# Performance work log

Hardware: AMD Instinct MI355X
Metric: run time of the kernel (lower is better)

## Reference

```python
import jax, jax.numpy as jnp
import numpy as np

NOISE_LEVEL = 0.05
GAMMA = 0.2  # dt/tau


def setup_inputs() -> dict:
    key = jax.random.key(0)
    ks = jax.random.split(key, 4)
    B, T, I, L, O = 64, 512, 128, 1024, 128
    return {
        "input": jax.random.normal(ks[0], (B, T, I), dtype=jnp.float32),
        "noise": jax.random.normal(ks[1], (B, T, L), dtype=jnp.float32),
        "wi": jax.random.normal(ks[2], (I, L), dtype=jnp.float32),
        "si": jnp.ones((I,), dtype=jnp.float32),
        "wrec": jax.random.normal(ks[3], (L, L), dtype=jnp.float32) * (1.0 / np.sqrt(L)),
        "b": jnp.zeros((L,), dtype=jnp.float32),
        "wo": jax.random.normal(jax.random.fold_in(key, 7), (L, O), dtype=jnp.float32) * (1.0 / L),
        "so": jnp.ones((O,), dtype=jnp.float32),
        "h0": jnp.zeros((L,), dtype=jnp.float32),
    }


def reference(input, noise, wi, si, wrec, b, wo, so, h0):
    B = input.shape[0]
    # proxy parameters: wi_full = (wi.T * si).T == wi * si[:, None]; wo_full = wo * so
    wi_full = wi * si[:, None]          # (I, L)
    wo_full = wo * so                   # (L, O)

    h_init = jnp.broadcast_to(h0, (B, h0.shape[0]))  # (B, L)
    r_init = jnp.tanh(h_init)

    # Precompute input projections for all steps (no sequential dependency).
    u = jnp.einsum('bti,il->btl', input, wi_full)     # (B, T, L)

    def step(carry, xs):
        h, r = carry
        u_t, n_t = xs                                 # (B, L), (B, L)
        h = h + NOISE_LEVEL * n_t + GAMMA * (-h + r @ wrec.T + u_t)
        r = jnp.tanh(h + b)
        out_t = jnp.tanh(h) @ wo_full                 # (B, O)
        return (h, r), out_t

    xs = (jnp.swapaxes(u, 0, 1), jnp.swapaxes(noise, 0, 1))  # time-major
    _, out_t = jax.lax.scan(step, (h_init, r_init), xs)
    return jnp.swapaxes(out_t, 0, 1)                 # (B, T, O)
```

## Files before the change

kernel.cpp:

```cpp
#include <hip/hip_runtime.h>
#include <hip/hip_bf16.h>
#include <cstdint>
#include <cstddef>


static constexpr int B = 64, T = 512, I = 128, L = 1024, O = 128;
static constexpr float C_NOISE = 0.05f, C_GAMMA = 0.2f;

static constexpr int NROW = 4, BT = 16, NJB = 16, JT = 64;

static constexpr size_t WREC_OFF = 0;
static constexpr size_t WIT_OFF  = WREC_OFF + (size_t)L * L * 2;
static constexpr size_t WOT_OFF  = WIT_OFF + (size_t)L * I * 2;
static constexpr size_t RBUF_OFF = WOT_OFF + (size_t)O * L * 2;
static constexpr size_t RBUF_BYTES = (size_t)2 * B * L * 2;
static constexpr size_t HBUF_OFF = ((RBUF_OFF + RBUF_BYTES + 131072 + 511) / 512) * 512;
static constexpr size_t WS_NEED  = HBUF_OFF + (size_t)B * T * L * 2;

typedef __attribute__((ext_vector_type(8))) short s16x8;
typedef __attribute__((ext_vector_type(4))) float f32x4;
typedef __attribute__((ext_vector_type(2))) unsigned long long u64x2;

__device__ __forceinline__ float fexp2(float x) {
#if __has_builtin(__builtin_amdgcn_exp2f)
  return __builtin_amdgcn_exp2f(x);
#else
  return exp2f(x);
#endif
}
__device__ __forceinline__ float frcp(float x) {
#if __has_builtin(__builtin_amdgcn_rcpf)
  return __builtin_amdgcn_rcpf(x);
#else
  return 1.0f / x;
#endif
}
__device__ __forceinline__ float fast_tanh(float x) {
  float e = fexp2(x * 2.8853900817779268f);
  return 1.0f - 2.0f * frcp(e + 1.0f);
}
__device__ __forceinline__ uint16_t bf16bits(float x) {
  __hip_bfloat16 h = __float2bfloat16(x);
  return *reinterpret_cast<uint16_t*>(&h);
}

__global__ void pack_kernel(const float* __restrict__ wi, const float* __restrict__ si,
                            const float* __restrict__ wrec,
                            const float* __restrict__ wo, const float* __restrict__ so,
                            uint8_t* __restrict__ ws) {
  int idx = blockIdx.x * blockDim.x + threadIdx.x;
  int stride = gridDim.x * blockDim.x;

  __hip_bfloat16* wrecb = (__hip_bfloat16*)(ws + WREC_OFF);
  for (int i = idx; i < L * L; i += stride) wrecb[i] = __float2bfloat16(wrec[i]);

  __hip_bfloat16* wit = (__hip_bfloat16*)(ws + WIT_OFF);
  for (int n = idx; n < L * I; n += stride) {
    int l = n >> 7, ii = n & 127;
    wit[n] = __float2bfloat16(wi[(size_t)ii * L + l] * si[ii]);
  }
  __hip_bfloat16* wot = (__hip_bfloat16*)(ws + WOT_OFF);
  for (int n = idx; n < O * L; n += stride) {
    int o = n >> 10, l = n & 1023;
    wot[n] = __float2bfloat16(wo[(size_t)l * O + o] * so[o]);
  }
  uint32_t* rb = (uint32_t*)(ws + RBUF_OFF);
  for (size_t n = idx; n < RBUF_BYTES / 4; n += stride) rb[n] = 0;
}

__launch_bounds__(256, 1)
__global__ void rnn_kernel(const float* __restrict__ input, const float* __restrict__ noise,
                           const float* __restrict__ bvec, const float* __restrict__ h0,
                           uint8_t* __restrict__ ws) {
  const int tid  = threadIdx.x;
  const int lane = tid & 63;
  const int w    = tid >> 6;
  const int bx   = blockIdx.x;
  const int row  = bx & 3;
  const int jblk = bx >> 2;
  const int b0   = row * BT;
  const int j0   = jblk * JT;
  const int l15  = lane & 15;
  const int lhi  = lane >> 4;

  const int jc0  = j0 + w * 16 + lhi * 4;
  const int mybatch = b0 + l15;

  const short* wrecb = (const short*)(ws + WREC_OFF);
  const short* wit   = (const short*)(ws + WIT_OFF);
  uint64_t* rbuf     = (uint64_t*)(ws + RBUF_OFF);
  __hip_bfloat16* hbuf = (__hip_bfloat16*)(ws + HBUF_OFF);

  __shared__ __align__(16) uint8_t ldsA[2][16 * 2048];

  s16x8 wfrag[32];
  #pragma unroll
  for (int kt = 0; kt < 32; ++kt)
    wfrag[kt] = *(const s16x8*)(wrecb + (size_t)(j0 + w * 16 + l15) * L + kt * 32 + lhi * 8);
  s16x8 wifrag[4];
  #pragma unroll
  for (int kt = 0; kt < 4; ++kt)
    wifrag[kt] = *(const s16x8*)(wit + (size_t)(j0 + w * 16 + l15) * I + kt * 32 + lhi * 8);

  f32x4 bias, h;
  #pragma unroll
  for (int q = 0; q < 4; ++q) { bias[q] = bvec[jc0 + q]; h[q] = h0[jc0 + q]; }

  const int grow = tid >> 4;
  const int gseg = tid & 15;
  const int gsw  = (grow ^ gseg) & 7;

  {
    uint64_t pv = 0;
    #pragma unroll
    for (int q = 0; q < 4; ++q)
      pv |= (uint64_t)bf16bits(fast_tanh(h0[jc0 + q])) << (16 * q);
    pv = (pv & ~1ull) | 1ull;
    size_t slot = (size_t)mybatch * (L / 4) + (size_t)(jc0 >> 2);
    __hip_atomic_store(&rbuf[slot], pv, __ATOMIC_RELAXED, __HIP_MEMORY_SCOPE_AGENT);
  }

  for (int t = 0; t < T; ++t) {
    f32x4 inLo[4], inHi[4];
    #pragma unroll
    for (int kt = 0; kt < 4; ++kt) {
      const float* p = input + ((size_t)(b0 + l15) * T + t) * I + kt * 32 + lhi * 8;
      inLo[kt] = *(const f32x4*)p;
      inHi[kt] = *(const f32x4*)(p + 4);
    }
    f32x4 nz = *(const f32x4*)(noise + ((size_t)mybatch * T + t) * L + jc0);
    s16x8 af[4];
    #pragma unroll
    for (int kt = 0; kt < 4; ++kt)
      #pragma unroll
      for (int q = 0; q < 4; ++q) {
        af[kt][q]     = (short)bf16bits(inLo[kt][q]);
        af[kt][q + 4] = (short)bf16bits(inHi[kt][q]);
      }

    f32x4 acc0 = {0.f,0.f,0.f,0.f}, acc1 = {0.f,0.f,0.f,0.f};
    f32x4 acc2 = {0.f,0.f,0.f,0.f}, acc3 = {0.f,0.f,0.f,0.f};
    acc0 = __builtin_amdgcn_mfma_f32_16x16x32_bf16(wifrag[0], af[0], acc0, 0, 0, 0);
    acc1 = __builtin_amdgcn_mfma_f32_16x16x32_bf16(wifrag[1], af[1], acc1, 0, 0, 0);
    acc2 = __builtin_amdgcn_mfma_f32_16x16x32_bf16(wifrag[2], af[2], acc2, 0, 0, 0);
    acc3 = __builtin_amdgcn_mfma_f32_16x16x32_bf16(wifrag[3], af[3], acc3, 0, 0, 0);

    u64x2 v[8];
    {
      const uint64_t want = (uint64_t)(((t >> 1) & 1) ^ 1);
      const uint8_t* src = (const uint8_t*)rbuf
                         + (size_t)(t & 1) * (B * L * 2)
                         + (size_t)(b0 + grow) * 2048 + (size_t)gseg * 128;
      uint32_t spin = 0;
      uint64_t bad;
      do {
        #pragma unroll
        for (int i = 0; i < 8; ++i)
          asm volatile("global_load_dwordx4 %0, %1, off sc0 sc1"
                       : "=&v"(v[i]) : "v"(src + i * 16) : "memory");
        asm volatile("s_waitcnt vmcnt(0)" ::: "memory");
        bad = 0;
        #pragma unroll
        for (int i = 0; i < 8; ++i)
          bad |= (v[i].x ^ want) | (v[i].y ^ want);
        bad &= 1ull;
      } while (bad && (++spin < (1u << 18)));
      __builtin_amdgcn_sched_barrier(0);
      uint8_t* dst = ldsA[t & 1] + grow * 2048 + gseg * 128;
      #pragma unroll
      for (int i = 0; i < 8; ++i)
        *(u64x2*)(dst + ((i ^ gsw) * 16)) = v[i];
    }
    __syncthreads();

    const uint8_t* Ab = ldsA[t & 1];
    #pragma unroll
    for (int kt = 0; kt < 32; ++kt) {
      int slot = ((kt * 4 + lhi) ^ ((l15 ^ (kt >> 1)) & 7)) * 16;
      s16x8 a = *(const s16x8*)(Ab + l15 * 2048 + slot);
      switch (kt & 3) {
        case 0: acc0 = __builtin_amdgcn_mfma_f32_16x16x32_bf16(wfrag[kt], a, acc0, 0, 0, 0); break;
        case 1: acc1 = __builtin_amdgcn_mfma_f32_16x16x32_bf16(wfrag[kt], a, acc1, 0, 0, 0); break;
        case 2: acc2 = __builtin_amdgcn_mfma_f32_16x16x32_bf16(wfrag[kt], a, acc2, 0, 0, 0); break;
        default: acc3 = __builtin_amdgcn_mfma_f32_16x16x32_bf16(wfrag[kt], a, acc3, 0, 0, 0); break;
      }
    }

    uint64_t pv = 0;
    #pragma unroll
    for (int q = 0; q < 4; ++q) {
      float hn = 0.8f * h[q] + C_GAMMA * ((acc0[q] + acc1[q]) + (acc2[q] + acc3[q]))
               + C_NOISE * nz[q];
      h[q] = hn;
      pv |= (uint64_t)bf16bits(fast_tanh(hn + bias[q])) << (16 * q);
    }
    {
      const uint64_t sb = (uint64_t)((((t + 1) >> 1) & 1) ^ 1);
      pv = (pv & ~1ull) | sb;
      size_t slot = (size_t)((t + 1) & 1) * (B * L / 4)
                  + (size_t)mybatch * (L / 4) + (size_t)(jc0 >> 2);
      __hip_atomic_store(&rbuf[slot], pv, __ATOMIC_RELAXED, __HIP_MEMORY_SCOPE_AGENT);
    }

    {
      uint64_t hv = 0;
      #pragma unroll
      for (int q = 0; q < 4; ++q)
        hv |= (uint64_t)bf16bits(fast_tanh(h[q])) << (16 * q);
      *(uint64_t*)(hbuf + ((size_t)mybatch * T + t) * L + jc0) = hv;
    }
  }
}

__launch_bounds__(256)
__global__ void out_gemm(const uint8_t* __restrict__ ws, float* __restrict__ out) {
  const short* hs  = (const short*)(ws + HBUF_OFF);
  const short* wot = (const short*)(ws + WOT_OFF);
  const int tid = threadIdx.x, lane = tid & 63, w = tid >> 6;
  const int wm = w >> 1, wn = w & 1;
  const int l15 = lane & 15, lhi = lane >> 4;
  const size_t m0 = (size_t)blockIdx.x * 128 + (size_t)wm * 64;

  f32x4 acc[4][4] = {};
  for (int kt = 0; kt < 32; ++kt) {
    s16x8 a[4], b[4];
    #pragma unroll
    for (int fi = 0; fi < 4; ++fi)
      a[fi] = *(const s16x8*)(hs + (m0 + fi * 16 + l15) * L + kt * 32 + lhi * 8);
    #pragma unroll
    for (int fj = 0; fj < 4; ++fj)
      b[fj] = *(const s16x8*)(wot + (size_t)(wn * 64 + fj * 16 + l15) * L + kt * 32 + lhi * 8);
    #pragma unroll
    for (int fi = 0; fi < 4; ++fi)
      #pragma unroll
      for (int fj = 0; fj < 4; ++fj)
        acc[fi][fj] = __builtin_amdgcn_mfma_f32_16x16x32_bf16(a[fi], b[fj], acc[fi][fj], 0, 0, 0);
  }
  #pragma unroll
  for (int fi = 0; fi < 4; ++fi)
    #pragma unroll
    for (int fj = 0; fj < 4; ++fj)
      #pragma unroll
      for (int q = 0; q < 4; ++q) {
        size_t m = m0 + fi * 16 + lhi * 4 + q;
        out[m * O + wn * 64 + fj * 16 + l15] = acc[fi][fj][q];
      }
}

__global__ void ws_too_small(float* out, int n) {
  int i = blockIdx.x * blockDim.x + threadIdx.x;
  if (i < n) out[i] = 12345.0f;
}

extern "C" void kernel_launch(void* const* d_in, const int* in_sizes, int n_in,
                              void* d_out, int out_size, void* d_ws, size_t ws_size,
                              hipStream_t stream) {
  const float* input = (const float*)d_in[0];
  const float* noise = (const float*)d_in[1];
  const float* wi    = (const float*)d_in[2];
  const float* si    = (const float*)d_in[3];
  const float* wrec  = (const float*)d_in[4];
  const float* bvec  = (const float*)d_in[5];
  const float* wo    = (const float*)d_in[6];
  const float* so    = (const float*)d_in[7];
  const float* h0    = (const float*)d_in[8];
  uint8_t* ws = (uint8_t*)d_ws;
  float* out = (float*)d_out;

  if (ws_size < WS_NEED) {
    ws_too_small<<<(out_size + 255) / 256, 256, 0, stream>>>(out, out_size);
    return;
  }

  pack_kernel<<<256, 256, 0, stream>>>(wi, si, wrec, wo, so, ws);
  rnn_kernel<<<NROW * NJB, 256, 0, stream>>>(input, noise, bvec, h0, ws);
  out_gemm<<<(B * T) / 128, 256, 0, stream>>>(ws, out);
}
```

Measured before the change: 2.052 ms.

## Replace persistent spin-synchronized RNN kernel with per-timestep kernel launches

The persistent recurrent kernel, which exchanged tanh state between blocks through flag-tagged global buffers and spin loops, is replaced by one kernel launch per time step. Hidden state is kept in a float workspace and ping-pong r buffers are selected on the host. This removes the spin-polling and flag encoding, but adds a kernel launch per step and reloads the recurrent weight fragments from memory on every step.

```diff
diff --git a/kernel.cpp b/kernel.cpp
--- a/kernel.cpp
+++ b/kernel.cpp
@@ -13,8 +13,8 @@
 static constexpr size_t WIT_OFF  = WREC_OFF + (size_t)L * L * 2;
 static constexpr size_t WOT_OFF  = WIT_OFF + (size_t)L * I * 2;
 static constexpr size_t RBUF_OFF = WOT_OFF + (size_t)O * L * 2;
-static constexpr size_t RBUF_BYTES = (size_t)2 * B * L * 2;
-static constexpr size_t HBUF_OFF = ((RBUF_OFF + RBUF_BYTES + 131072 + 511) / 512) * 512;
+static constexpr size_t HST_OFF  = RBUF_OFF + (size_t)2 * B * L * 2;
+static constexpr size_t HBUF_OFF = ((HST_OFF + (size_t)B * L * 4 + 511) / 512) * 512;
 static constexpr size_t WS_NEED  = HBUF_OFF + (size_t)B * T * L * 2;
 
 typedef __attribute__((ext_vector_type(8))) short s16x8;
@@ -47,6 +47,7 @@
 __global__ void pack_kernel(const float* __restrict__ wi, const float* __restrict__ si,
                             const float* __restrict__ wrec,
                             const float* __restrict__ wo, const float* __restrict__ so,
+                            const float* __restrict__ h0,
                             uint8_t* __restrict__ ws) {
   int idx = blockIdx.x * blockDim.x + threadIdx.x;
   int stride = gridDim.x * blockDim.x;
@@ -64,14 +65,20 @@
     int o = n >> 10, l = n & 1023;
     wot[n] = __float2bfloat16(wo[(size_t)l * O + o] * so[o]);
   }
-  uint32_t* rb = (uint32_t*)(ws + RBUF_OFF);
-  for (size_t n = idx; n < RBUF_BYTES / 4; n += stride) rb[n] = 0;
+  uint16_t* r0 = (uint16_t*)(ws + RBUF_OFF);
+  float* hst = (float*)(ws + HST_OFF);
+  for (int n = idx; n < B * L; n += stride) {
+    float hv = h0[n & 1023];
+    r0[n] = bf16bits(fast_tanh(hv));
+    hst[n] = hv;
+  }
 }
 
 __launch_bounds__(256, 1)
-__global__ void rnn_kernel(const float* __restrict__ input, const float* __restrict__ noise,
-                           const float* __restrict__ bvec, const float* __restrict__ h0,
-                           uint8_t* __restrict__ ws) {
+__global__ void step_kernel(const float* __restrict__ input, const float* __restrict__ noise,
+                            const float* __restrict__ bvec, uint8_t* __restrict__ ws,
+                            const uint16_t* __restrict__ rsrc, uint16_t* __restrict__ rdst,
+                            int t) {
   const int tid  = threadIdx.x;
   const int lane = tid & 63;
   const int w    = tid >> 6;
@@ -88,10 +95,20 @@
 
   const short* wrecb = (const short*)(ws + WREC_OFF);
   const short* wit   = (const short*)(ws + WIT_OFF);
-  uint64_t* rbuf     = (uint64_t*)(ws + RBUF_OFF);
+  float* hstate      = (float*)(ws + HST_OFF);
   __hip_bfloat16* hbuf = (__hip_bfloat16*)(ws + HBUF_OFF);
 
-  __shared__ __align__(16) uint8_t ldsA[2][16 * 2048];
+  __shared__ __align__(16) uint8_t ldsA[16 * 2048];
+
+  const int grow = tid >> 4;
+  const int gseg = tid & 15;
+  const int gsw  = (grow ^ gseg) & 7;
+  u64x2 v[8];
+  {
+    const uint8_t* src = (const uint8_t*)rsrc + (size_t)(b0 + grow) * 2048 + (size_t)gseg * 128;
+    #pragma unroll
+    for (int i = 0; i < 8; ++i) v[i] = *(const u64x2*)(src + i * 16);
+  }
 
   s16x8 wfrag[32];
   #pragma unroll
@@ -102,114 +119,65 @@
   for (int kt = 0; kt < 4; ++kt)
     wifrag[kt] = *(const s16x8*)(wit + (size_t)(j0 + w * 16 + l15) * I + kt * 32 + lhi * 8);
 
-  f32x4 bias, h;
-  #pragma unroll
-  for (int q = 0; q < 4; ++q) { bias[q] = bvec[jc0 + q]; h[q] = h0[jc0 + q]; }
-
-  const int grow = tid >> 4;
-  const int gseg = tid & 15;
-  const int gsw  = (grow ^ gseg) & 7;
+  f32x4 inLo[4], inHi[4];
+  #pragma unroll
+  for (int kt = 0; kt < 4; ++kt) {
+    const float* p = input + ((size_t)mybatch * T + t) * I + kt * 32 + lhi * 8;
+    inLo[kt] = *(const f32x4*)p;
+    inHi[kt] = *(const f32x4*)(p + 4);
+  }
+  f32x4 nz = *(const f32x4*)(noise + ((size_t)mybatch * T + t) * L + jc0);
+  f32x4 bias = *(const f32x4*)(bvec + jc0);
+  f32x4 hv = *(const f32x4*)(hstate + (size_t)mybatch * L + jc0);
+  s16x8 af[4];
+  #pragma unroll
+  for (int kt = 0; kt < 4; ++kt)
+    #pragma unroll
+    for (int q = 0; q < 4; ++q) {
+      af[kt][q]     = (short)bf16bits(inLo[kt][q]);
+      af[kt][q + 4] = (short)bf16bits(inHi[kt][q]);
+    }
 
   {
-    uint64_t pv = 0;
-    #pragma unroll
-    for (int q = 0; q < 4; ++q)
-      pv |= (uint64_t)bf16bits(fast_tanh(h0[jc0 + q])) << (16 * q);
-    pv = (pv & ~1ull) | 1ull;
-    size_t slot = (size_t)mybatch * (L / 4) + (size_t)(jc0 >> 2);
-    __hip_atomic_store(&rbuf[slot], pv, __ATOMIC_RELAXED, __HIP_MEMORY_SCOPE_AGENT);
-  }
-
-  for (int t = 0; t < T; ++t) {
-    f32x4 inLo[4], inHi[4];
-    #pragma unroll
-    for (int kt = 0; kt < 4; ++kt) {
-      const float* p = input + ((size_t)(b0 + l15) * T + t) * I + kt * 32 + lhi * 8;
-      inLo[kt] = *(const f32x4*)p;
-      inHi[kt] = *(const f32x4*)(p + 4);
+    uint8_t* dst = ldsA + grow * 2048 + gseg * 128;
+    #pragma unroll
+    for (int i = 0; i < 8; ++i)
+      *(u64x2*)(dst + ((i ^ gsw) * 16)) = v[i];
+  }
+
+  f32x4 acc0 = {0.f,0.f,0.f,0.f}, acc1 = {0.f,0.f,0.f,0.f};
+  f32x4 acc2 = {0.f,0.f,0.f,0.f}, acc3 = {0.f,0.f,0.f,0.f};
+  acc0 = __builtin_amdgcn_mfma_f32_16x16x32_bf16(wifrag[0], af[0], acc0, 0, 0, 0);
+  acc1 = __builtin_amdgcn_mfma_f32_16x16x32_bf16(wifrag[1], af[1], acc1, 0, 0, 0);
+  acc2 = __builtin_amdgcn_mfma_f32_16x16x32_bf16(wifrag[2], af[2], acc2, 0, 0, 0);
+  acc3 = __builtin_amdgcn_mfma_f32_16x16x32_bf16(wifrag[3], af[3], acc3, 0, 0, 0);
+
+  __syncthreads();
+
+  #pragma unroll
+  for (int kt = 0; kt < 32; ++kt) {
+    int slot = ((kt * 4 + lhi) ^ ((l15 ^ (kt >> 1)) & 7)) * 16;
+    s16x8 a = *(const s16x8*)(ldsA + l15 * 2048 + slot);
+    switch (kt & 3) {
+      case 0: acc0 = __builtin_amdgcn_mfma_f32_16x16x32_bf16(wfrag[kt], a, acc0, 0, 0, 0); break;
+      case 1: acc1 = __builtin_amdgcn_mfma_f32_16x16x32_bf16(wfrag[kt], a, acc1, 0, 0, 0); break;
+      case 2: acc2 = __builtin_amdgcn_mfma_f32_16x16x32_bf16(wfrag[kt], a, acc2, 0, 0, 0); break;
+      default: acc3 = __builtin_amdgcn_mfma_f32_16x16x32_bf16(wfrag[kt], a, acc3, 0, 0, 0); break;
     }
-    f32x4 nz = *(const f32x4*)(noise + ((size_t)mybatch * T + t) * L + jc0);
-    s16x8 af[4];
-    #pragma unroll
-    for (int kt = 0; kt < 4; ++kt)
-      #pragma unroll
-      for (int q = 0; q < 4; ++q) {
-        af[kt][q]     = (short)bf16bits(inLo[kt][q]);
-        af[kt][q + 4] = (short)bf16bits(inHi[kt][q]);
-      }
-
-    f32x4 acc0 = {0.f,0.f,0.f,0.f}, acc1 = {0.f,0.f,0.f,0.f};
-    f32x4 acc2 = {0.f,0.f,0.f,0.f}, acc3 = {0.f,0.f,0.f,0.f};
-    acc0 = __builtin_amdgcn_mfma_f32_16x16x32_bf16(wifrag[0], af[0], acc0, 0, 0, 0);
-    acc1 = __builtin_amdgcn_mfma_f32_16x16x32_bf16(wifrag[1], af[1], acc1, 0, 0, 0);
-    acc2 = __builtin_amdgcn_mfma_f32_16x16x32_bf16(wifrag[2], af[2], acc2, 0, 0, 0);
-    acc3 = __builtin_amdgcn_mfma_f32_16x16x32_bf16(wifrag[3], af[3], acc3, 0, 0, 0);
-
-    u64x2 v[8];
-    {
-      const uint64_t want = (uint64_t)(((t >> 1) & 1) ^ 1);
-      const uint8_t* src = (const uint8_t*)rbuf
-                         + (size_t)(t & 1) * (B * L * 2)
-                         + (size_t)(b0 + grow) * 2048 + (size_t)gseg * 128;
-      uint32_t spin = 0;
-      uint64_t bad;
-      do {
-        #pragma unroll
-        for (int i = 0; i < 8; ++i)
-          asm volatile("global_load_dwordx4 %0, %1, off sc0 sc1"
-                       : "=&v"(v[i]) : "v"(src + i * 16) : "memory");
-        asm volatile("s_waitcnt vmcnt(0)" ::: "memory");
-        bad = 0;
-        #pragma unroll
-        for (int i = 0; i < 8; ++i)
-          bad |= (v[i].x ^ want) | (v[i].y ^ want);
-        bad &= 1ull;
-      } while (bad && (++spin < (1u << 18)));
-      __builtin_amdgcn_sched_barrier(0);
-      uint8_t* dst = ldsA[t & 1] + grow * 2048 + gseg * 128;
-      #pragma unroll
-      for (int i = 0; i < 8; ++i)
-        *(u64x2*)(dst + ((i ^ gsw) * 16)) = v[i];
-    }
-    __syncthreads();
-
-    const uint8_t* Ab = ldsA[t & 1];
-    #pragma unroll
-    for (int kt = 0; kt < 32; ++kt) {
-      int slot = ((kt * 4 + lhi) ^ ((l15 ^ (kt >> 1)) & 7)) * 16;
-      s16x8 a = *(const s16x8*)(Ab + l15 * 2048 + slot);
-      switch (kt & 3) {
-        case 0: acc0 = __builtin_amdgcn_mfma_f32_16x16x32_bf16(wfrag[kt], a, acc0, 0, 0, 0); break;
-        case 1: acc1 = __builtin_amdgcn_mfma_f32_16x16x32_bf16(wfrag[kt], a, acc1, 0, 0, 0); break;
-        case 2: acc2 = __builtin_amdgcn_mfma_f32_16x16x32_bf16(wfrag[kt], a, acc2, 0, 0, 0); break;
-        default: acc3 = __builtin_amdgcn_mfma_f32_16x16x32_bf16(wfrag[kt], a, acc3, 0, 0, 0); break;
-      }
-    }
-
-    uint64_t pv = 0;
-    #pragma unroll
-    for (int q = 0; q < 4; ++q) {
-      float hn = 0.8f * h[q] + C_GAMMA * ((acc0[q] + acc1[q]) + (acc2[q] + acc3[q]))
-               + C_NOISE * nz[q];
-      h[q] = hn;
-      pv |= (uint64_t)bf16bits(fast_tanh(hn + bias[q])) << (16 * q);
-    }
-    {
-      const uint64_t sb = (uint64_t)((((t + 1) >> 1) & 1) ^ 1);
-      pv = (pv & ~1ull) | sb;
-      size_t slot = (size_t)((t + 1) & 1) * (B * L / 4)
-                  + (size_t)mybatch * (L / 4) + (size_t)(jc0 >> 2);
-      __hip_atomic_store(&rbuf[slot], pv, __ATOMIC_RELAXED, __HIP_MEMORY_SCOPE_AGENT);
-    }
-
-    {
-      uint64_t hv = 0;
-      #pragma unroll
-      for (int q = 0; q < 4; ++q)
-        hv |= (uint64_t)bf16bits(fast_tanh(h[q])) << (16 * q);
-      *(uint64_t*)(hbuf + ((size_t)mybatch * T + t) * L + jc0) = hv;
-    }
-  }
+  }
+
+  uint64_t pv = 0, hvout = 0;
+  #pragma unroll
+  for (int q = 0; q < 4; ++q) {
+    float hn = 0.8f * hv[q] + C_GAMMA * ((acc0[q] + acc1[q]) + (acc2[q] + acc3[q]))
+             + C_NOISE * nz[q];
+    hv[q] = hn;
+    pv    |= (uint64_t)bf16bits(fast_tanh(hn + bias[q])) << (16 * q);
+    hvout |= (uint64_t)bf16bits(fast_tanh(hn)) << (16 * q);
+  }
+  *(f32x4*)(hstate + (size_t)mybatch * L + jc0) = hv;
+  *(uint64_t*)(rdst + (size_t)mybatch * L + jc0) = pv;
+  *(uint64_t*)(hbuf + ((size_t)mybatch * T + t) * L + jc0) = hvout;
 }
 
 __launch_bounds__(256)
@@ -272,7 +240,15 @@
     return;
   }
 
-  pack_kernel<<<256, 256, 0, stream>>>(wi, si, wrec, wo, so, ws);
-  rnn_kernel<<<NROW * NJB, 256, 0, stream>>>(input, noise, bvec, h0, ws);
+  pack_kernel<<<256, 256, 0, stream>>>(wi, si, wrec, wo, so, h0, ws);
+
+  uint16_t* r0 = (uint16_t*)(ws + RBUF_OFF);
+  uint16_t* r1 = r0 + (size_t)B * L;
+  for (int t = 0; t < T; ++t) {
+    const uint16_t* rs = (t & 1) ? r1 : r0;
+    uint16_t*       rd = (t & 1) ? r0 : r1;
+    step_kernel<<<NROW * NJB, 256, 0, stream>>>(input, noise, bvec, ws, rs, rd, t);
+  }
+
   out_gemm<<<(B * T) / 128, 256, 0, stream>>>(ws, out);
 }
```

New measurement: 4.127 ms. +101.1%, slower.
